# Kernel optimization log

Measured on AMD Instinct MI355X. Metric: run time of the kernel, lower is better.

The kernel has to match this reference:

```python
import jax, jax.numpy as jnp
import numpy as np

B, L, D, H = 2, 2048, 2048, 16
DH = D // H  # 128


def setup_inputs() -> dict:
    key = jax.random.key(0)
    k1, k2 = jax.random.split(key)
    inputs = jax.random.normal(k1, (B, L, D), dtype=jnp.float32)
    # additive causal mask: 0 on/below diagonal, -inf above (matches typical usage)
    neg = jnp.finfo(jnp.float32).min
    causal = jnp.where(jnp.tril(jnp.ones((L, L), dtype=bool)), 0.0, neg)
    attn_mask = causal[None, None, :, :].astype(jnp.float32)
    # torch Linear(d, 3d, bias=False): y = x @ W.T; here W_qkv is stored as [d, 3d]
    W_qkv = jax.random.normal(k2, (D, 3 * D), dtype=jnp.float32) * (1.0 / np.sqrt(D))
    return {"inputs": inputs, "attn_mask": attn_mask, "W_qkv": W_qkv}


def reference(inputs, attn_mask, W_qkv):
    b, l, d = inputs.shape
    qkv = inputs @ W_qkv                       # [B, L, 3D]
    qkv = qkv.reshape(b, l, H, 3 * DH)         # [B, L, H, 3*dh]
    qkv = qkv.transpose(0, 2, 1, 3)            # [B, H, L, 3*dh]
    Q, K, V = jnp.split(qkv, 3, axis=-1)       # each [B, H, L, dh]
    scale = jnp.sqrt(jnp.float32(DH))
    scores = jnp.einsum("bhqd,bhkd->bhqk", Q, K) / scale
    scores = scores + attn_mask
    probs = jax.nn.softmax(scores, axis=-1)    # dropout is identity in eval / p=0
    out = jnp.einsum("bhqk,bhkd->bhqd", probs, V)
    out = out.transpose(0, 2, 1, 3).reshape(b, l, d)
    return out
```

## Files before the change

kernel.cpp:

```cpp
#include <hip/hip_runtime.h>

#define SEQL 2048
#define NHEAD 16
#define N3 6144
#define KDIM 2048

typedef __attribute__((ext_vector_type(8))) short bf16x8;
typedef __attribute__((ext_vector_type(4))) float f32x4;
typedef __attribute__((ext_vector_type(16))) float f32x16;
typedef __attribute__((ext_vector_type(4))) unsigned short us4;
typedef __attribute__((ext_vector_type(4))) float fl4;
typedef __attribute__((ext_vector_type(4))) unsigned int u32x4;

__device__ __forceinline__ unsigned short f2bf(float x) {
    unsigned u = __builtin_bit_cast(unsigned, x);
    u += 0x7fffu + ((u >> 16) & 1u);
    return (unsigned short)(u >> 16);
}

__device__ __forceinline__ void gload16(const void* g, void* l) {
    __builtin_amdgcn_global_load_lds(
        (const __attribute__((address_space(1))) unsigned int*)g,
        (__attribute__((address_space(3))) unsigned int*)l,
        16, 0, 0);
}

__device__ __forceinline__ unsigned cvtpk_bf16(float lo, float hi) {
    unsigned r;
    asm("v_cvt_pk_bf16_f32 %0, %1, %2" : "=v"(r) : "v"(lo), "v"(hi));
    return r;
}
__device__ __forceinline__ void plane32_swap(unsigned &a, unsigned &b) {
    asm("v_permlane32_swap_b32 %0, %1" : "+v"(a), "+v"(b));
}

__global__ __launch_bounds__(256) void k_prep(const float* __restrict__ X,
                                              const float* __restrict__ W,
                                              unsigned short* __restrict__ Xb,
                                              unsigned short* __restrict__ Wt) {
    __shared__ alignas(16) unsigned short Ts[64 * 68];
    int bid = blockIdx.x, t = threadIdx.x;
    if (bid < 2048) {
        int tid = bid * 256 + t;
        const fl4* in4 = (const fl4*)X;
        us4* out4 = (us4*)Xb;
#pragma unroll
        for (int j = 0; j < 4; ++j) {
            int idx = tid + j * 524288;
            fl4 v = in4[idx];
            us4 o;
            o.x = f2bf(v.x); o.y = f2bf(v.y); o.z = f2bf(v.z); o.w = f2bf(v.w);
            out4[idx] = o;
        }
    } else {
        int b2 = bid - 2048;
        int n0 = (b2 % 96) * 64, k0 = (b2 / 96) * 64;
        int r = t >> 2, c4 = t & 3;
#pragma unroll
        for (int j = 0; j < 4; ++j) {
            int c = (c4 + j * 4) * 4;
            fl4 v = *(const fl4*)&W[(size_t)(k0 + r) * N3 + n0 + c];
            Ts[r * 68 + c + 0] = f2bf(v.x);
            Ts[r * 68 + c + 1] = f2bf(v.y);
            Ts[r * 68 + c + 2] = f2bf(v.z);
            Ts[r * 68 + c + 3] = f2bf(v.w);
        }
        __syncthreads();
#pragma unroll
        for (int j = 0; j < 2; ++j) {
            int chunk = c4 + j * 4;
#pragma unroll
            for (int h = 0; h < 2; ++h) {
                us4 o;
                o.x = Ts[(chunk * 8 + h * 4 + 0) * 68 + r];
                o.y = Ts[(chunk * 8 + h * 4 + 1) * 68 + r];
                o.z = Ts[(chunk * 8 + h * 4 + 2) * 68 + r];
                o.w = Ts[(chunk * 8 + h * 4 + 3) * 68 + r];
                *(us4*)&Wt[(size_t)(n0 + r) * KDIM + k0 + chunk * 8 + h * 4] = o;
            }
        }
    }
}

__global__ __launch_bounds__(512, 2) void k_gemm_qkv(const unsigned short* __restrict__ Xb,
                                                     const unsigned short* __restrict__ Wt,
                                                     unsigned short* __restrict__ Qb,
                                                     unsigned short* __restrict__ Kb,
                                                     unsigned short* __restrict__ Vt) {
    __shared__ alignas(16) char smem[131072];
    int t = threadIdx.x;
    int wid = t >> 6, lane = t & 63, g = lane >> 4, l15 = lane & 15;
    int bid = blockIdx.x;
    bid = (bid & 7) * 48 + (bid >> 3);
    int tmi = bid & 15, tni = bid >> 4;
    int tm = tmi * 256, tn = tni * 256;
    const unsigned short* Abase = Xb + (size_t)tm * KDIM;
    const unsigned short* Bbase = Wt + (size_t)tn * KDIM;
    int wm = wid >> 2, wn = wid & 3;
    f32x4 acc[8][4];
#pragma unroll
    for (int i = 0; i < 8; ++i)
#pragma unroll
        for (int j = 0; j < 4; ++j) acc[i][j] = (f32x4){0.f, 0.f, 0.f, 0.f};

    auto stage_a = [&](int tile) {
        int k0 = tile * 32;
        char* dst = smem + (tile & 3) * 32768;
#pragma unroll
        for (int j = 0; j < 2; ++j) {
            int p = j * 8192 + t * 16;
            int s = p >> 4;
            int mr = s >> 3;
            int sl = (s & 7) ^ (mr & 7);
            int m = mr * 2 + (sl >> 2);
            gload16(Abase + (size_t)m * KDIM + k0 + (sl & 3) * 8,
                    dst + j * 8192 + wid * 1024);
        }
    };
    auto stage_b = [&](int tile) {
        int k0 = tile * 32;
        char* dst = smem + (tile & 3) * 32768 + 16384;
#pragma unroll
        for (int j = 0; j < 2; ++j) {
            int p = j * 8192 + t * 16;
            int s = p >> 4;
            int nr = s >> 3;
            int sl = (s & 7) ^ (nr & 7);
            int n = nr * 2 + (sl >> 2);
            gload16(Bbase + (size_t)n * KDIM + k0 + (sl & 3) * 8,
                    dst + j * 8192 + wid * 1024);
        }
    };

    stage_a(0); stage_b(0); stage_a(1); stage_b(1); stage_a(2); stage_b(2);
    asm volatile("s_waitcnt vmcnt(8)" ::: "memory");
    __builtin_amdgcn_s_barrier();
    asm volatile("" ::: "memory");

    auto iter = [&](int tt, int pf, int vm) {
        const char* Abuf = smem + (tt & 3) * 32768;
        const char* Bbuf = Abuf + 16384;
        bf16x8 bfv[4];
#pragma unroll
        for (int mh = 0; mh < 2; ++mh) {
            bf16x8 af[4];
#pragma unroll
            for (int q = 0; q < 4; ++q) {
                int ra = wm * 128 + mh * 64 + q * 16 + l15;
                int mr = ra >> 1;
                af[q] = *(const bf16x8*)(Abuf + mr * 128 +
                        ((((ra & 1) * 4 + g) ^ (mr & 7)) << 4));
            }
            if (mh == 0) {
#pragma unroll
                for (int bj = 0; bj < 4; ++bj) {
                    int rb = wn * 64 + bj * 16 + l15;
                    int nr = rb >> 1;
                    bfv[bj] = *(const bf16x8*)(Bbuf + nr * 128 +
                              ((((rb & 1) * 4 + g) ^ (nr & 7)) << 4));
                }
                if (pf >= 0) stage_a(pf);
            } else {
                if (pf >= 0) stage_b(pf);
            }
            asm volatile("" ::: "memory");
            __builtin_amdgcn_s_barrier();
            __builtin_amdgcn_s_setprio(1);
#pragma unroll
            for (int q = 0; q < 4; ++q)
#pragma unroll
                for (int bj = 0; bj < 4; ++bj)
                    acc[mh * 4 + q][bj] = __builtin_amdgcn_mfma_f32_16x16x32_bf16(
                        af[q], bfv[bj], acc[mh * 4 + q][bj], 0, 0, 0);
            __builtin_amdgcn_s_setprio(0);
            asm volatile("" ::: "memory");
            if (mh == 1) {
                if (vm == 8)      asm volatile("s_waitcnt vmcnt(8)" ::: "memory");
                else if (vm == 4) asm volatile("s_waitcnt vmcnt(4)" ::: "memory");
                else if (vm == 0) asm volatile("s_waitcnt vmcnt(0)" ::: "memory");
            }
            __builtin_amdgcn_s_barrier();
            asm volatile("" ::: "memory");
        }
    };

    for (int tt = 0; tt < 61; ++tt) iter(tt, tt + 3, 8);
    iter(61, -1, 4);
    iter(62, -1, 0);
    iter(63, -1, -1);

    int b = tm >> 11, lp0 = tm & 2047;
    const float qsc = 0.08838834764831845f * 1.44269504089f;
    int half_w = wn >> 1;
    int tyw = (tni * 2 + half_w) % 3;
    char* Tw = smem + half_w * 65536;
#pragma unroll
    for (int fi = 0; fi < 8; ++fi)
#pragma unroll
        for (int bj = 0; bj < 4; ++bj) {
            int d = wn * 64 + bj * 16 + l15;
            int dl = d & 127;
#pragma unroll
            for (int r = 0; r < 4; ++r) {
                int mm = wm * 128 + fi * 16 + g * 4 + r;
                float v = acc[fi][bj][r];
                unsigned short bv = f2bf(tyw == 0 ? v * qsc : v);
                int byte;
                if (tyw == 2)
                    byte = dl * 512 + ((((mm >> 3) ^ (dl & 31)) & 31) << 4) + (mm & 7) * 2;
                else
                    byte = mm * 256 + ((((dl >> 3) ^ (mm & 15)) & 15) << 4) + (dl & 7) * 2;
                *(unsigned short*)(Tw + byte) = bv;
            }
        }
    __syncthreads();
#pragma unroll
    for (int half = 0; half < 2; ++half) {
        int ty = (tni * 2 + half) % 3;
        int h  = (tni * 2 + half) / 3;
        const char* Tr = smem + half * 65536;
        if (ty == 2) {
#pragma unroll
            for (int c = 0; c < 8; ++c) {
                int id = c * 512 + t;
                int dl = id >> 5, Lc = id & 31;
                bf16x8 vv = *(const bf16x8*)(Tr + dl * 512 + (((Lc ^ (dl & 31)) & 31) << 4));
                int kt = (lp0 >> 6) + (Lc >> 3);
                *(bf16x8*)&Vt[(size_t)((b * NHEAD + h) * 32 + kt) * 8192 + dl * 64 +
                              (Lc & 7) * 8] = vv;
            }
        } else {
            unsigned short* dst = (ty == 0) ? Qb : Kb;
#pragma unroll
            for (int c = 0; c < 8; ++c) {
                int id = c * 512 + t;
                int mm = id >> 4, cc = id & 15;
                bf16x8 vv = *(const bf16x8*)(Tr + mm * 256 + (((cc ^ (mm & 15)) & 15) << 4));
                *(bf16x8*)&dst[((size_t)(b * NHEAD + h) * SEQL + lp0 + mm) * 128 + cc * 8] = vv;
            }
        }
    }
}

__global__ __launch_bounds__(256) void k_attn(const unsigned short* __restrict__ Qb,
                                              const unsigned short* __restrict__ Kb,
                                              const unsigned short* __restrict__ Vt,
                                              float* __restrict__ out) {
    __shared__ alignas(16) unsigned short Ks[64 * 128];
    __shared__ alignas(16) unsigned short Vs[128 * 64];
    __shared__ float Fx[4][32];
    int t = threadIdx.x, w = t >> 6, lane = t & 63;
    int l31 = lane & 31, hi = lane >> 5;
    int qi = 15 - (int)blockIdx.x;
    int bh = blockIdx.y;
    int qb = qi * 128;
    int qg = qb + w * 32 + l31;
    int qwmin = qb + w * 32, qwmax = qwmin + 31;

    bf16x8 qf[8];
    const unsigned short* Qp = Qb + (size_t)(bh * SEQL + qg) * 128;
#pragma unroll
    for (int ks = 0; ks < 8; ++ks)
        qf[ks] = *(const bf16x8*)(Qp + ks * 16 + hi * 8);

    f32x16 accO[4];
#pragma unroll
    for (int db = 0; db < 4; ++db)
#pragma unroll
        for (int e = 0; e < 16; ++e) accO[db][e] = 0.f;
    float mstate = -3.0e38f, lsum = 0.f;

    int nkv = 2 * qi + 2;
    for (int kt = 0; kt < nkv; ++kt) {
        int kv0 = kt * 64;
#pragma unroll
        for (int j = 0; j < 4; ++j) {
            int p = j * 4096 + t * 16;
            int rk = p >> 8;
            int sk = ((p >> 4) & 15) ^ (rk & 15);
            gload16(Kb + (size_t)(bh * SEQL + kv0 + rk) * 128 + sk * 8,
                    (char*)Ks + j * 4096 + w * 1024);
            int rv = p >> 7;
            int sv = ((p >> 4) & 7) ^ (rv & 7);
            gload16(Vt + ((size_t)(bh * 32 + (kv0 >> 6)) * 128 + rv) * 64 + sv * 8,
                    (char*)Vs + j * 4096 + w * 1024);
        }
        __syncthreads();

        if (kv0 <= qwmax) {
            f32x16 s[2];
#pragma unroll
            for (int blk = 0; blk < 2; ++blk)
#pragma unroll
                for (int e = 0; e < 16; ++e) s[blk][e] = 0.f;
#pragma unroll
            for (int ks = 0; ks < 8; ++ks) {
                int c = ks * 2 + hi;
#pragma unroll
                for (int blk = 0; blk < 2; ++blk) {
                    int row = blk * 32 + l31;
                    bf16x8 kf = *(const bf16x8*)((const char*)Ks + row * 256 +
                                                 (((c ^ (row & 15)) & 15) << 4));
                    s[blk] = __builtin_amdgcn_mfma_f32_32x32x16_bf16(kf, qf[ks], s[blk], 0, 0, 0);
                }
            }
            if (kv0 + 63 > qwmin) {
#pragma unroll
                for (int blk = 0; blk < 2; ++blk)
#pragma unroll
                    for (int r = 0; r < 16; ++r) {
                        int kvg = kv0 + blk * 32 + (r & 3) + 8 * (r >> 2) + 4 * hi;
                        if (kvg > qg) s[blk][r] = -3.0e38f;
                    }
            }
            float tmax = -3.0e38f;
#pragma unroll
            for (int blk = 0; blk < 2; ++blk)
#pragma unroll
                for (int r = 0; r < 16; ++r) tmax = fmaxf(tmax, s[blk][r]);
            tmax = fmaxf(tmax, __shfl_xor(tmax, 32));
            if (__any(tmax > mstate + 8.0f)) {
                float mnew = fmaxf(mstate, tmax);
                float fs = __builtin_amdgcn_exp2f(mstate - mnew);
                lsum *= fs;
                mstate = mnew;
                Fx[w][l31] = fs;
                f32x4 fv[4];
#pragma unroll
                for (int q4 = 0; q4 < 4; ++q4)
                    fv[q4] = *(const f32x4*)&Fx[w][q4 * 8 + 4 * hi];
#pragma unroll
                for (int db = 0; db < 4; ++db)
#pragma unroll
                    for (int r = 0; r < 16; ++r)
                        accO[db][r] *= fv[r >> 2][r & 3];
            }
            float ps = 0.f;
#pragma unroll
            for (int blk = 0; blk < 2; ++blk)
#pragma unroll
                for (int r = 0; r < 16; ++r) {
                    float p = __builtin_amdgcn_exp2f(s[blk][r] - mstate);
                    s[blk][r] = p;
                    ps += p;
                }
            ps += __shfl_xor(ps, 32);
            lsum += ps;
            unsigned pa[4][4];
#pragma unroll
            for (int blk = 0; blk < 2; ++blk)
#pragma unroll
                for (int hf = 0; hf < 2; ++hf) {
                    int o = hf * 8;
                    unsigned d0 = cvtpk_bf16(s[blk][o + 0], s[blk][o + 1]);
                    unsigned d2 = cvtpk_bf16(s[blk][o + 4], s[blk][o + 5]);
                    plane32_swap(d0, d2);
                    unsigned d1 = cvtpk_bf16(s[blk][o + 2], s[blk][o + 3]);
                    unsigned d3 = cvtpk_bf16(s[blk][o + 6], s[blk][o + 7]);
                    plane32_swap(d1, d3);
                    pa[blk * 2 + hf][0] = d0; pa[blk * 2 + hf][1] = d1;
                    pa[blk * 2 + hf][2] = d2; pa[blk * 2 + hf][3] = d3;
                }
#pragma unroll
            for (int ksv = 0; ksv < 4; ++ksv) {
                u32x4 pu = {pa[ksv][0], pa[ksv][1], pa[ksv][2], pa[ksv][3]};
                bf16x8 paf = __builtin_bit_cast(bf16x8, pu);
                int c = ksv * 2 + hi;
#pragma unroll
                for (int db = 0; db < 4; ++db) {
                    int rv = db * 32 + l31;
                    bf16x8 vf = *(const bf16x8*)((const char*)Vs + rv * 128 +
                                                 (((c ^ (rv & 7)) & 7) << 4));
                    accO[db] = __builtin_amdgcn_mfma_f32_32x32x16_bf16(paf, vf, accO[db], 0, 0, 0);
                }
            }
        }
        __syncthreads();
    }
    float inv = 1.0f / lsum;
    Fx[w][l31] = inv;
    f32x4 iv[4];
#pragma unroll
    for (int q4 = 0; q4 < 4; ++q4)
        iv[q4] = *(const f32x4*)&Fx[w][q4 * 8 + 4 * hi];
    int b = bh >> 4, h = bh & 15;
    float* ob = out + (size_t)(b * SEQL + qb + w * 32) * 2048 + h * 128;
#pragma unroll
    for (int db = 0; db < 4; ++db)
#pragma unroll
        for (int r = 0; r < 16; ++r) {
            int qr = (r & 3) + 8 * (r >> 2) + 4 * hi;
            ob[(size_t)qr * 2048 + db * 32 + l31] = accO[db][r] * iv[r >> 2][r & 3];
        }
}

extern "C" void kernel_launch(void* const* d_in, const int* in_sizes, int n_in,
                              void* d_out, int out_size, void* d_ws, size_t ws_size,
                              hipStream_t stream) {
    const float* x = (const float*)d_in[0];
    const float* w = (const float*)d_in[2];
    float* out = (float*)d_out;
    char* ws = (char*)d_ws;
    unsigned short* Xb = (unsigned short*)(ws);
    unsigned short* Wt = (unsigned short*)(ws + 16777216);
    unsigned short* Qb = (unsigned short*)(ws + 41943040);
    unsigned short* Kb = (unsigned short*)(ws + 58720256);
    unsigned short* Vt = (unsigned short*)(ws + 75497472);

    hipLaunchKernelGGL(k_prep, dim3(5120), dim3(256), 0, stream, x, w, Xb, Wt);
    hipLaunchKernelGGL(k_gemm_qkv, dim3(384), dim3(512), 0, stream, Xb, Wt, Qb, Kb, Vt);
    hipLaunchKernelGGL(k_attn, dim3(16, 32), dim3(256), 0, stream, Qb, Kb, Vt, out);
}
```

Before: 363.3 us.

## Shrink QKV GEMM tile to 128x256 with double-buffered LDS for higher occupancy

The QKV projection GEMM tile drops from 256x256 to 128x256 and the grid doubles to 768 blocks. The LDS pipeline goes from a 4-stage buffer (131 KB) to a 2-stage double buffer (64 KB), and load addresses and fragment offsets are precomputed outside the K loop. The launch bound is raised to 4 blocks per CU. The aim is better occupancy and load balance across CUs, at the cost of less data reuse per tile and a shallower prefetch depth.

```diff
diff --git a/kernel.cpp b/kernel.cpp
--- a/kernel.cpp
+++ b/kernel.cpp
@@ -82,132 +82,108 @@
     }
 }
 
-__global__ __launch_bounds__(512, 2) void k_gemm_qkv(const unsigned short* __restrict__ Xb,
+__global__ __launch_bounds__(512, 4) void k_gemm_qkv(const unsigned short* __restrict__ Xb,
                                                      const unsigned short* __restrict__ Wt,
                                                      unsigned short* __restrict__ Qb,
                                                      unsigned short* __restrict__ Kb,
                                                      unsigned short* __restrict__ Vt) {
-    __shared__ alignas(16) char smem[131072];
+    __shared__ alignas(16) char smem[65536];
     int t = threadIdx.x;
     int wid = t >> 6, lane = t & 63, g = lane >> 4, l15 = lane & 15;
     int bid = blockIdx.x;
-    bid = (bid & 7) * 48 + (bid >> 3);
-    int tmi = bid & 15, tni = bid >> 4;
-    int tm = tmi * 256, tn = tni * 256;
+    bid = (bid & 7) * 96 + (bid >> 3);
+    int tmi = bid & 31, tni = bid >> 5;
+    int tm = tmi * 128, tn = tni * 256;
     const unsigned short* Abase = Xb + (size_t)tm * KDIM;
     const unsigned short* Bbase = Wt + (size_t)tn * KDIM;
     int wm = wid >> 2, wn = wid & 3;
-    f32x4 acc[8][4];
-#pragma unroll
-    for (int i = 0; i < 8; ++i)
+
+    int mrA = t >> 3, psA = t & 7;
+    int slA = psA ^ (mrA & 7);
+    const unsigned short* a_src = Abase + (size_t)(mrA * 2 + (slA >> 2)) * KDIM + (slA & 3) * 8;
+    int nr0 = t >> 3, sl0 = (t & 7) ^ (nr0 & 7);
+    const unsigned short* b_src0 = Bbase + (size_t)(nr0 * 2 + (sl0 >> 2)) * KDIM + (sl0 & 3) * 8;
+    int nr1 = 64 + (t >> 3), sl1 = (t & 7) ^ (nr1 & 7);
+    const unsigned short* b_src1 = Bbase + (size_t)(nr1 * 2 + (sl1 >> 2)) * KDIM + (sl1 & 3) * 8;
+    int awoff = wid * 1024 + lane * 16;
+
+    int offA[4], offB[4];
+#pragma unroll
+    for (int q = 0; q < 4; ++q) {
+        int ra = wm * 64 + q * 16 + l15;
+        int mr = ra >> 1;
+        offA[q] = mr * 128 + ((((ra & 1) * 4 + g) ^ (mr & 7)) << 4);
+        int rb = wn * 64 + q * 16 + l15;
+        int nr = rb >> 1;
+        offB[q] = nr * 128 + ((((rb & 1) * 4 + g) ^ (nr & 7)) << 4);
+    }
+
+    f32x4 acc[4][4];
+#pragma unroll
+    for (int i = 0; i < 4; ++i)
 #pragma unroll
         for (int j = 0; j < 4; ++j) acc[i][j] = (f32x4){0.f, 0.f, 0.f, 0.f};
 
-    auto stage_a = [&](int tile) {
+    auto STAGE = [&](int tile) {
         int k0 = tile * 32;
-        char* dst = smem + (tile & 3) * 32768;
-#pragma unroll
-        for (int j = 0; j < 2; ++j) {
-            int p = j * 8192 + t * 16;
-            int s = p >> 4;
-            int mr = s >> 3;
-            int sl = (s & 7) ^ (mr & 7);
-            int m = mr * 2 + (sl >> 2);
-            gload16(Abase + (size_t)m * KDIM + k0 + (sl & 3) * 8,
-                    dst + j * 8192 + wid * 1024);
-        }
+        char* base = smem + (tile & 1) * 24576;
+        gload16(a_src + k0, base + awoff);
+        gload16(b_src0 + k0, base + 8192 + awoff);
+        gload16(b_src1 + k0, base + 16384 + awoff);
     };
-    auto stage_b = [&](int tile) {
-        int k0 = tile * 32;
-        char* dst = smem + (tile & 3) * 32768 + 16384;
-#pragma unroll
-        for (int j = 0; j < 2; ++j) {
-            int p = j * 8192 + t * 16;
-            int s = p >> 4;
-            int nr = s >> 3;
-            int sl = (s & 7) ^ (nr & 7);
-            int n = nr * 2 + (sl >> 2);
-            gload16(Bbase + (size_t)n * KDIM + k0 + (sl & 3) * 8,
-                    dst + j * 8192 + wid * 1024);
-        }
-    };
-
-    stage_a(0); stage_b(0); stage_a(1); stage_b(1); stage_a(2); stage_b(2);
-    asm volatile("s_waitcnt vmcnt(8)" ::: "memory");
+
+    STAGE(0); STAGE(1);
+    asm volatile("s_waitcnt vmcnt(3)" ::: "memory");
     __builtin_amdgcn_s_barrier();
     asm volatile("" ::: "memory");
 
-    auto iter = [&](int tt, int pf, int vm) {
-        const char* Abuf = smem + (tt & 3) * 32768;
-        const char* Bbuf = Abuf + 16384;
-        bf16x8 bfv[4];
-#pragma unroll
-        for (int mh = 0; mh < 2; ++mh) {
-            bf16x8 af[4];
-#pragma unroll
-            for (int q = 0; q < 4; ++q) {
-                int ra = wm * 128 + mh * 64 + q * 16 + l15;
-                int mr = ra >> 1;
-                af[q] = *(const bf16x8*)(Abuf + mr * 128 +
-                        ((((ra & 1) * 4 + g) ^ (mr & 7)) << 4));
-            }
-            if (mh == 0) {
-#pragma unroll
-                for (int bj = 0; bj < 4; ++bj) {
-                    int rb = wn * 64 + bj * 16 + l15;
-                    int nr = rb >> 1;
-                    bfv[bj] = *(const bf16x8*)(Bbuf + nr * 128 +
-                              ((((rb & 1) * 4 + g) ^ (nr & 7)) << 4));
-                }
-                if (pf >= 0) stage_a(pf);
-            } else {
-                if (pf >= 0) stage_b(pf);
-            }
-            asm volatile("" ::: "memory");
-            __builtin_amdgcn_s_barrier();
-            __builtin_amdgcn_s_setprio(1);
-#pragma unroll
-            for (int q = 0; q < 4; ++q)
-#pragma unroll
-                for (int bj = 0; bj < 4; ++bj)
-                    acc[mh * 4 + q][bj] = __builtin_amdgcn_mfma_f32_16x16x32_bf16(
-                        af[q], bfv[bj], acc[mh * 4 + q][bj], 0, 0, 0);
-            __builtin_amdgcn_s_setprio(0);
-            asm volatile("" ::: "memory");
-            if (mh == 1) {
-                if (vm == 8)      asm volatile("s_waitcnt vmcnt(8)" ::: "memory");
-                else if (vm == 4) asm volatile("s_waitcnt vmcnt(4)" ::: "memory");
-                else if (vm == 0) asm volatile("s_waitcnt vmcnt(0)" ::: "memory");
-            }
-            __builtin_amdgcn_s_barrier();
-            asm volatile("" ::: "memory");
-        }
-    };
-
-    for (int tt = 0; tt < 61; ++tt) iter(tt, tt + 3, 8);
-    iter(61, -1, 4);
-    iter(62, -1, 0);
-    iter(63, -1, -1);
+    for (int tt = 0; tt < 64; ++tt) {
+        const char* base = smem + (tt & 1) * 24576;
+        bf16x8 af[4], bfv[4];
+#pragma unroll
+        for (int q = 0; q < 4; ++q) {
+            af[q]  = *(const bf16x8*)(base + offA[q]);
+            bfv[q] = *(const bf16x8*)(base + 8192 + offB[q]);
+        }
+        __builtin_amdgcn_s_setprio(1);
+#pragma unroll
+        for (int i = 0; i < 4; ++i)
+#pragma unroll
+            for (int j = 0; j < 4; ++j)
+                acc[i][j] = __builtin_amdgcn_mfma_f32_16x16x32_bf16(
+                    af[i], bfv[j], acc[i][j], 0, 0, 0);
+        __builtin_amdgcn_s_setprio(0);
+        asm volatile("" ::: "memory");
+        __builtin_amdgcn_s_barrier();
+        asm volatile("" ::: "memory");
+        if (tt < 62) {
+            STAGE(tt + 2);
+            asm volatile("s_waitcnt vmcnt(3)" ::: "memory");
+        } else if (tt == 62) {
+            asm volatile("s_waitcnt vmcnt(0)" ::: "memory");
+        }
+        __builtin_amdgcn_s_barrier();
+        asm volatile("" ::: "memory");
+    }
 
     int b = tm >> 11, lp0 = tm & 2047;
     const float qsc = 0.08838834764831845f * 1.44269504089f;
     int half_w = wn >> 1;
-    int tyw = (tni * 2 + half_w) % 3;
-    char* Tw = smem + half_w * 65536;
-#pragma unroll
-    for (int fi = 0; fi < 8; ++fi)
+    int tyw = (2 * tni + half_w) % 3;
+    char* Tw = smem + half_w * 32768;
+#pragma unroll
+    for (int fi = 0; fi < 4; ++fi)
 #pragma unroll
         for (int bj = 0; bj < 4; ++bj) {
-            int d = wn * 64 + bj * 16 + l15;
-            int dl = d & 127;
+            int dl = (wn & 1) * 64 + bj * 16 + l15;
 #pragma unroll
             for (int r = 0; r < 4; ++r) {
-                int mm = wm * 128 + fi * 16 + g * 4 + r;
+                int mm = wm * 64 + fi * 16 + g * 4 + r;
                 float v = acc[fi][bj][r];
                 unsigned short bv = f2bf(tyw == 0 ? v * qsc : v);
                 int byte;
                 if (tyw == 2)
-                    byte = dl * 512 + ((((mm >> 3) ^ (dl & 31)) & 31) << 4) + (mm & 7) * 2;
+                    byte = dl * 256 + ((((mm >> 3) ^ (dl & 15)) & 15) << 4) + (mm & 7) * 2;
                 else
                     byte = mm * 256 + ((((dl >> 3) ^ (mm & 15)) & 15) << 4) + (dl & 7) * 2;
                 *(unsigned short*)(Tw + byte) = bv;
@@ -216,27 +192,27 @@
     __syncthreads();
 #pragma unroll
     for (int half = 0; half < 2; ++half) {
-        int ty = (tni * 2 + half) % 3;
-        int h  = (tni * 2 + half) / 3;
-        const char* Tr = smem + half * 65536;
+        int ty = (2 * tni + half) % 3;
+        int hh = (tni * 256 + half * 128) / 384;
+        const char* Tr = smem + half * 32768;
         if (ty == 2) {
 #pragma unroll
-            for (int c = 0; c < 8; ++c) {
-                int id = c * 512 + t;
-                int dl = id >> 5, Lc = id & 31;
-                bf16x8 vv = *(const bf16x8*)(Tr + dl * 512 + (((Lc ^ (dl & 31)) & 31) << 4));
-                int kt = (lp0 >> 6) + (Lc >> 3);
-                *(bf16x8*)&Vt[(size_t)((b * NHEAD + h) * 32 + kt) * 8192 + dl * 64 +
-                              (Lc & 7) * 8] = vv;
+            for (int i = 0; i < 4; ++i) {
+                int id = i * 512 + t;
+                int dv = id >> 4, c2 = id & 15;
+                bf16x8 vv = *(const bf16x8*)(Tr + dv * 256 + (((c2 ^ (dv & 15)) & 15) << 4));
+                int kt = (lp0 >> 6) + (c2 >> 3);
+                *(bf16x8*)&Vt[(size_t)((b * NHEAD + hh) * 32 + kt) * 8192 + dv * 64 +
+                              (c2 & 7) * 8] = vv;
             }
         } else {
             unsigned short* dst = (ty == 0) ? Qb : Kb;
 #pragma unroll
-            for (int c = 0; c < 8; ++c) {
-                int id = c * 512 + t;
+            for (int i = 0; i < 4; ++i) {
+                int id = i * 512 + t;
                 int mm = id >> 4, cc = id & 15;
                 bf16x8 vv = *(const bf16x8*)(Tr + mm * 256 + (((cc ^ (mm & 15)) & 15) << 4));
-                *(bf16x8*)&dst[((size_t)(b * NHEAD + h) * SEQL + lp0 + mm) * 128 + cc * 8] = vv;
+                *(bf16x8*)&dst[((size_t)(b * NHEAD + hh) * SEQL + lp0 + mm) * 128 + cc * 8] = vv;
             }
         }
     }
@@ -408,6 +384,6 @@
     unsigned short* Vt = (unsigned short*)(ws + 75497472);
 
     hipLaunchKernelGGL(k_prep, dim3(5120), dim3(256), 0, stream, x, w, Xb, Wt);
-    hipLaunchKernelGGL(k_gemm_qkv, dim3(384), dim3(512), 0, stream, Xb, Wt, Qb, Kb, Vt);
+    hipLaunchKernelGGL(k_gemm_qkv, dim3(768), dim3(512), 0, stream, Xb, Wt, Qb, Kb, Vt);
     hipLaunchKernelGGL(k_attn, dim3(16, 32), dim3(256), 0, stream, Qb, Kb, Vt, out);
 }
```

Result: no change. 362.6 us (-0.2%).
